# Kernel tuning notes

Hardware: AMD Instinct MI355X
Metric: run time of the kernel (lower is better)

## Reference

```python
import jax, jax.numpy as jnp
import numpy as np

N_PATCHES = 10
PATCH = 100
RECEPTIVE_FIELD = 0
N_SCALES = 2


def setup_inputs() -> dict:
    key = jax.random.key(0)
    k1, k2, k3, k4 = jax.random.split(key, 4)
    B, HL, WL, HH, WH = 8, 112, 112, 1024, 1024
    x_lows = jax.random.normal(k1, (N_SCALES, B, HL, WL, 3), jnp.float32)
    x_highs = jax.random.normal(k2, (N_SCALES, B, HH, WH, 3), jnp.float32)
    ats_map = jax.random.uniform(k3, (B, HL, WL), jnp.float32)
    ats_index = jax.random.randint(k4, (B, HL, WL), 0, N_SCALES).astype(jnp.int32)
    scales = jnp.array([1.0, 2.0], jnp.float32)
    return dict(x_lows=x_lows, x_highs=x_highs, ats_map=ats_map,
                ats_index=ats_index, scales=scales)


def _extract_patches(img, cy, cx):
    # img [H,W,3]; cy, cx [N] int32 -> [N,P,P,3] patch gather (vmapped dynamic_slice)
    def one(c):
        return jax.lax.dynamic_slice(img, (c[0], c[1], 0), (PATCH, PATCH, 3))
    return jax.vmap(one)(jnp.stack([cy, cx], axis=-1))


def _forward(x_lows, x_highs, ats_map, ats_index, scales):
    B, HL, WL = ats_map.shape
    HH, WH = x_highs.shape[2], x_highs.shape[3]
    # --- categorical sampling without replacement (Gumbel top-k) over flat attention
    att = ats_map.reshape(B, -1)
    att = att / att.sum(axis=-1, keepdims=True)
    gkey = jax.random.key(1)
    u = jax.random.uniform(gkey, (B, HL * WL))
    gumbel = -jnp.log(-jnp.log(u + 1e-10) + 1e-10)
    _, idx = jax.lax.top_k(jnp.log(att + 1e-10) + gumbel, N_PATCHES)  # [B,N]
    sampled_att = jnp.take_along_axis(att, idx, axis=1)               # [B,N]
    sy = (idx // WL).astype(jnp.float32)
    sx = (idx % WL).astype(jnp.float32)
    samples = jnp.stack([sy, sx], axis=-1)                            # [B,N,2]
    # per-sample scale routing: gather scale id at sampled locations
    res_index = jnp.take_along_axis(ats_index.reshape(B, -1), idx, axis=1)  # [B,N]
    # map low-res grid coords -> high-res top-left corners
    ratio = jnp.array([(HH - PATCH) / (HL - 1.0), (WH - PATCH) / (WL - 1.0)], jnp.float32)
    hi_max = jnp.array([HH - PATCH, WH - PATCH], jnp.int32)
    patches = jnp.zeros((B, N_PATCHES, PATCH, PATCH, 3), jnp.float32)
    samples_out = samples
    for s in range(N_SCALES):  # small static loop over scales (mirrors original)
        coords = samples / scales[s]                                   # divide both dims by scale
        corner = jnp.clip(jnp.round(coords * ratio).astype(jnp.int32), 0, hi_max)
        patches_s = jax.vmap(_extract_patches)(x_highs[s], corner[..., 0], corner[..., 1])
        mask = (res_index == s)                                        # [B,N]
        patches = jnp.where(mask[..., None, None, None], patches_s, patches)
        samples_out = jnp.where(mask[..., None], coords, samples_out)
    offsets = jnp.zeros_like(samples) + RECEPTIVE_FIELD / 2.0
    return patches, sampled_att, offsets, samples_out


def reference(x_lows, x_highs, ats_map, ats_index, scales):
    return _forward(x_lows, x_highs, ats_map, ats_index, scales)
```

## Files before the change

kernel.cpp:

```cpp
#include <hip/hip_runtime.h>
#include <math.h>

#define NPATCHES 10
#define PATCH    100
#define NSCALES  2
#define BB       8
#define HL       112
#define WL       112
#define HH       1024
#define WH       1024
#define HW       (HL*WL)
#define WSLICE   784
#define NW       16

__device__ __forceinline__ unsigned rotl32(unsigned x, unsigned r){
  return (x << r) | (x >> (32u - r));
}

__device__ __forceinline__ void threefry2x32_key01(unsigned x0, unsigned x1,
                                                   unsigned &o0, unsigned &o1){
  const unsigned ks0 = 0u;
  const unsigned ks1 = 1u;
  const unsigned ks2 = 0x1BD11BDAu ^ ks0 ^ ks1;
  unsigned a = x0 + ks0;
  unsigned b = x1 + ks1;
#define TF_RND(r) { a += b; b = rotl32(b, (r)); b ^= a; }
  TF_RND(13u) TF_RND(15u) TF_RND(26u) TF_RND(6u)
  a += ks1; b += ks2 + 1u;
  TF_RND(17u) TF_RND(29u) TF_RND(16u) TF_RND(24u)
  a += ks2; b += ks0 + 2u;
  TF_RND(13u) TF_RND(15u) TF_RND(26u) TF_RND(6u)
  a += ks0; b += ks1 + 3u;
  TF_RND(17u) TF_RND(29u) TF_RND(16u) TF_RND(24u)
  a += ks1; b += ks2 + 4u;
  TF_RND(13u) TF_RND(15u) TF_RND(26u) TF_RND(6u)
  a += ks2; b += ks0 + 5u;
#undef TF_RND
  o0 = a; o1 = b;
}

__global__ __launch_bounds__(1024)
void msp_topk_kernel(const float* __restrict__ ats_map,
                     const int*   __restrict__ ats_index,
                     const float* __restrict__ scales,
                     float* __restrict__ out,
                     int*   __restrict__ ws)
{
  __shared__ float swv[NW];
  __shared__ float cand_v[NW * NPATCHES];
  __shared__ int   cand_i[NW * NPATCHES];
  __shared__ float s_sum;
  __shared__ int   sel[NPATCHES];

  const int b = blockIdx.x;
  const int t = threadIdx.x;
  const int w = t >> 6;
  const int l = t & 63;
  const int base = w * WSLICE;
  const float* am = ats_map + (size_t)b * HW;

  float a[13];
  float ps = 0.0f;
  #pragma unroll
  for (int j = 0; j < 13; ++j){
    const int off = l + 64 * j;
    float x = 0.0f;
    if (off < WSLICE) x = am[base + off];
    a[j] = x;
    ps += x;
  }
  for (int d = 32; d > 0; d >>= 1) ps += __shfl_down(ps, d, 64);
  if (l == 0) swv[w] = ps;
  __syncthreads();
  if (t == 0){
    float s = 0.0f;
    for (int k = 0; k < NW; ++k) s += swv[k];
    s_sum = s;
  }
  __syncthreads();
  const float S = s_sum;

  #pragma unroll
  for (int j = 0; j < 13; ++j){
    const int off = l + 64 * j;
    const int i = base + off;
    unsigned o0, o1;
    threefry2x32_key01(0u, (unsigned)(b * HW + i), o0, o1);
    const unsigned bits = o0 ^ o1;
    const float u = __uint_as_float((bits >> 9) | 0x3f800000u) - 1.0f;
    const float g = -logf(-logf(u + 1e-10f) + 1e-10f);
    const float att = a[j] / S;
    const float sc = logf(att + 1e-10f) + g;
    a[j] = (off < WSLICE) ? sc : -INFINITY;
  }

  float lv = -INFINITY; int lj = 0;
  #pragma unroll
  for (int j = 0; j < 13; ++j) if (a[j] > lv){ lv = a[j]; lj = j; }

  for (int n = 0; n < NPATCHES; ++n){
    float bv = lv;
    int   bi = (lv == -INFINITY) ? 0x7fffffff : (base + l + 64 * lj);
    for (int d = 32; d > 0; d >>= 1){
      const float v2 = __shfl_down(bv, d, 64);
      const int   i2 = __shfl_down(bi, d, 64);
      if (v2 > bv || (v2 == bv && i2 < bi)){ bv = v2; bi = i2; }
    }
    bv = __shfl(bv, 0, 64);
    bi = __shfl(bi, 0, 64);
    if (l == 0){ cand_v[w * NPATCHES + n] = bv; cand_i[w * NPATCHES + n] = bi; }
    const int rel = bi - base;
    if (bi != 0x7fffffff && (rel & 63) == l){
      a[rel >> 6] = -INFINITY;
      lv = -INFINITY; lj = 0;
      #pragma unroll
      for (int j = 0; j < 13; ++j) if (a[j] > lv){ lv = a[j]; lj = j; }
    }
  }
  __syncthreads();

  if (w == 0){
    float mv[3]; int mi[3];
    #pragma unroll
    for (int c = 0; c < 3; ++c){
      const int id = l + 64 * c;
      if (id < NW * NPATCHES){ mv[c] = cand_v[id]; mi[c] = cand_i[id]; }
      else { mv[c] = -INFINITY; mi[c] = 0x7fffffff; }
    }
    float cv = -INFINITY; int ci = 0x7fffffff;
    #pragma unroll
    for (int c = 0; c < 3; ++c)
      if (mv[c] > cv || (mv[c] == cv && mi[c] < ci)){ cv = mv[c]; ci = mi[c]; }

    for (int n = 0; n < NPATCHES; ++n){
      float bv = cv; int bi = ci;
      for (int d = 32; d > 0; d >>= 1){
        const float v2 = __shfl_down(bv, d, 64);
        const int   i2 = __shfl_down(bi, d, 64);
        if (v2 > bv || (v2 == bv && i2 < bi)){ bv = v2; bi = i2; }
      }
      bv = __shfl(bv, 0, 64);
      bi = __shfl(bi, 0, 64);
      if (l == 0) sel[n] = bi;
      bool had = false;
      #pragma unroll
      for (int c = 0; c < 3; ++c) if (mi[c] == bi && mv[c] == bv){ mv[c] = -INFINITY; had = true; }
      if (had){
        cv = -INFINITY; ci = 0x7fffffff;
        #pragma unroll
        for (int c = 0; c < 3; ++c)
          if (mv[c] > cv || (mv[c] == cv && mi[c] < ci)){ cv = mv[c]; ci = mi[c]; }
      }
    }
  }
  __syncthreads();

  if (t < NPATCHES){
    const int n = t;
    const int idx = sel[n];
    const float att = am[idx] / S;
    const int iy = idx / WL;
    const float sy = (float)iy;
    const float sx = (float)(idx - iy * WL);
    const int si = ats_index[(size_t)b * HW + idx];
    const float sc = scales[si];
    const float cy = sy / sc;
    const float cx = sx / sc;
    const float ratio = (float)(924.0 / 111.0);
    int corner_y = (int)rintf(cy * ratio);
    int corner_x = (int)rintf(cx * ratio);
    corner_y = min(max(corner_y, 0), HH - PATCH);
    corner_x = min(max(corner_x, 0), WH - PATCH);

    float* out_att = out + (size_t)BB * NPATCHES * PATCH * PATCH * 3;
    float* out_off = out_att + BB * NPATCHES;
    float* out_smp = out_off + BB * NPATCHES * 2;
    out_att[b * NPATCHES + n] = att;
    out_off[(b * NPATCHES + n) * 2 + 0] = 0.0f;
    out_off[(b * NPATCHES + n) * 2 + 1] = 0.0f;
    out_smp[(b * NPATCHES + n) * 2 + 0] = cy;
    out_smp[(b * NPATCHES + n) * 2 + 1] = cx;

    int* wsp = ws + (b * NPATCHES + n) * 4;
    wsp[0] = corner_y; wsp[1] = corner_x; wsp[2] = si; wsp[3] = 0;
  }
}

__global__ __launch_bounds__(256)
void msp_gather_kernel(const float* __restrict__ x_highs,
                       const int*   __restrict__ ws,
                       float* __restrict__ out)
{
  const int pn    = blockIdx.x;
  const int chunk = blockIdx.y;
  const int t = threadIdx.x;
  const int* w = ws + pn * 4;
  const int cy = w[0], cx = w[1], s = w[2];
  const int b = pn / NPATCHES;
  const float* src = x_highs + (size_t)(s * BB + b) * HH * (WH * 3);
  float* dst = out + (size_t)pn * (PATCH * PATCH * 3);
  const int begin = chunk * 20 * PATCH * 3;
  const int end   = begin + 20 * PATCH * 3;
  for (int f = begin + t; f < end; f += 256){
    const int row = f / (PATCH * 3);
    const int col = f - row * (PATCH * 3);
    dst[f] = src[(size_t)(cy + row) * (WH * 3) + (size_t)cx * 3 + col];
  }
}

extern "C" void kernel_launch(void* const* d_in, const int* in_sizes, int n_in,
                              void* d_out, int out_size, void* d_ws, size_t ws_size,
                              hipStream_t stream)
{
  const float* x_highs   = (const float*)d_in[1];
  const float* ats_map   = (const float*)d_in[2];
  const int*   ats_index = (const int*)d_in[3];
  const float* scales    = (const float*)d_in[4];
  float* out = (float*)d_out;
  int*   ws  = (int*)d_ws;

  hipLaunchKernelGGL(msp_topk_kernel, dim3(BB), dim3(1024), 0, stream,
                     ats_map, ats_index, scales, out, ws);
  hipLaunchKernelGGL(msp_gather_kernel, dim3(BB * NPATCHES, 5), dim3(256), 0, stream,
                     x_highs, ws, out);
}
```

Baseline: 40.61 us.

## Fuse top-k sampling and patch gather into one kernel per patch

Merges the top-k selection kernel and the patch-gather kernel into a single launch with one 1024-thread block per (batch, patch). Each block redundantly recomputes the Gumbel top-k for its batch, then copies only its own patch using 4-wide stores. This removes a second launch and the workspace round trip, at the cost of running the top-k computation ten times over (once per patch) and having fewer gather blocks.

```diff
diff --git a/kernel.cpp b/kernel.cpp
--- a/kernel.cpp
+++ b/kernel.cpp
@@ -3,7 +3,6 @@
 
 #define NPATCHES 10
 #define PATCH    100
-#define NSCALES  2
 #define BB       8
 #define HL       112
 #define WL       112
@@ -40,22 +39,25 @@
 }
 
 __global__ __launch_bounds__(1024)
-void msp_topk_kernel(const float* __restrict__ ats_map,
-                     const int*   __restrict__ ats_index,
-                     const float* __restrict__ scales,
-                     float* __restrict__ out,
-                     int*   __restrict__ ws)
+void msp_fused_kernel(const float* __restrict__ x_highs,
+                      const float* __restrict__ ats_map,
+                      const int*   __restrict__ ats_index,
+                      const float* __restrict__ scales,
+                      float* __restrict__ out)
 {
   __shared__ float swv[NW];
   __shared__ float cand_v[NW * NPATCHES];
   __shared__ int   cand_i[NW * NPATCHES];
   __shared__ float s_sum;
   __shared__ int   sel[NPATCHES];
-
-  const int b = blockIdx.x;
-  const int t = threadIdx.x;
-  const int w = t >> 6;
-  const int l = t & 63;
+  __shared__ int   c_cy, c_cx, c_si;
+
+  const int pn = blockIdx.x;
+  const int b  = pn / NPATCHES;
+  const int n  = pn - b * NPATCHES;
+  const int t  = threadIdx.x;
+  const int w  = t >> 6;
+  const int l  = t & 63;
   const int base = w * WSLICE;
   const float* am = ats_map + (size_t)b * HW;
 
@@ -98,7 +100,7 @@
   #pragma unroll
   for (int j = 0; j < 13; ++j) if (a[j] > lv){ lv = a[j]; lj = j; }
 
-  for (int n = 0; n < NPATCHES; ++n){
+  for (int k = 0; k < NPATCHES; ++k){
     float bv = lv;
     int   bi = (lv == -INFINITY) ? 0x7fffffff : (base + l + 64 * lj);
     for (int d = 32; d > 0; d >>= 1){
@@ -108,7 +110,7 @@
     }
     bv = __shfl(bv, 0, 64);
     bi = __shfl(bi, 0, 64);
-    if (l == 0){ cand_v[w * NPATCHES + n] = bv; cand_i[w * NPATCHES + n] = bi; }
+    if (l == 0){ cand_v[w * NPATCHES + k] = bv; cand_i[w * NPATCHES + k] = bi; }
     const int rel = bi - base;
     if (bi != 0x7fffffff && (rel & 63) == l){
       a[rel >> 6] = -INFINITY;
@@ -132,7 +134,7 @@
     for (int c = 0; c < 3; ++c)
       if (mv[c] > cv || (mv[c] == cv && mi[c] < ci)){ cv = mv[c]; ci = mi[c]; }
 
-    for (int n = 0; n < NPATCHES; ++n){
+    for (int k = 0; k < NPATCHES; ++k){
       float bv = cv; int bi = ci;
       for (int d = 32; d > 0; d >>= 1){
         const float v2 = __shfl_down(bv, d, 64);
@@ -141,7 +143,7 @@
       }
       bv = __shfl(bv, 0, 64);
       bi = __shfl(bi, 0, 64);
-      if (l == 0) sel[n] = bi;
+      if (l == 0) sel[k] = bi;
       bool had = false;
       #pragma unroll
       for (int c = 0; c < 3; ++c) if (mi[c] == bi && mv[c] == bv){ mv[c] = -INFINITY; had = true; }
@@ -155,8 +157,7 @@
   }
   __syncthreads();
 
-  if (t < NPATCHES){
-    const int n = t;
+  if (t == 0){
     const int idx = sel[n];
     const float att = am[idx] / S;
     const int iy = idx / WL;
@@ -164,47 +165,36 @@
     const float sx = (float)(idx - iy * WL);
     const int si = ats_index[(size_t)b * HW + idx];
     const float sc = scales[si];
-    const float cy = sy / sc;
-    const float cx = sx / sc;
+    const float cyf = sy / sc;
+    const float cxf = sx / sc;
     const float ratio = (float)(924.0 / 111.0);
-    int corner_y = (int)rintf(cy * ratio);
-    int corner_x = (int)rintf(cx * ratio);
+    int corner_y = (int)rintf(cyf * ratio);
+    int corner_x = (int)rintf(cxf * ratio);
     corner_y = min(max(corner_y, 0), HH - PATCH);
     corner_x = min(max(corner_x, 0), WH - PATCH);
 
     float* out_att = out + (size_t)BB * NPATCHES * PATCH * PATCH * 3;
     float* out_off = out_att + BB * NPATCHES;
     float* out_smp = out_off + BB * NPATCHES * 2;
-    out_att[b * NPATCHES + n] = att;
-    out_off[(b * NPATCHES + n) * 2 + 0] = 0.0f;
-    out_off[(b * NPATCHES + n) * 2 + 1] = 0.0f;
-    out_smp[(b * NPATCHES + n) * 2 + 0] = cy;
-    out_smp[(b * NPATCHES + n) * 2 + 1] = cx;
-
-    int* wsp = ws + (b * NPATCHES + n) * 4;
-    wsp[0] = corner_y; wsp[1] = corner_x; wsp[2] = si; wsp[3] = 0;
-  }
-}
-
-__global__ __launch_bounds__(256)
-void msp_gather_kernel(const float* __restrict__ x_highs,
-                       const int*   __restrict__ ws,
-                       float* __restrict__ out)
-{
-  const int pn    = blockIdx.x;
-  const int chunk = blockIdx.y;
-  const int t = threadIdx.x;
-  const int* w = ws + pn * 4;
-  const int cy = w[0], cx = w[1], s = w[2];
-  const int b = pn / NPATCHES;
-  const float* src = x_highs + (size_t)(s * BB + b) * HH * (WH * 3);
+    out_att[pn] = att;
+    out_off[pn * 2 + 0] = 0.0f;
+    out_off[pn * 2 + 1] = 0.0f;
+    out_smp[pn * 2 + 0] = cyf;
+    out_smp[pn * 2 + 1] = cxf;
+
+    c_cy = corner_y; c_cx = corner_x; c_si = si;
+  }
+  __syncthreads();
+
+  const int cy = c_cy, cx = c_cx, s = c_si;
+  const float* src = x_highs + (size_t)(s * BB + b) * ((size_t)HH * (WH * 3));
   float* dst = out + (size_t)pn * (PATCH * PATCH * 3);
-  const int begin = chunk * 20 * PATCH * 3;
-  const int end   = begin + 20 * PATCH * 3;
-  for (int f = begin + t; f < end; f += 256){
-    const int row = f / (PATCH * 3);
-    const int col = f - row * (PATCH * 3);
-    dst[f] = src[(size_t)(cy + row) * (WH * 3) + (size_t)cx * 3 + col];
+  for (int f = t * 4; f < PATCH * PATCH * 3; f += 4096){
+    const int row = f / 300;
+    const int col = f - row * 300;
+    const float* sp = src + (size_t)(cy + row) * (WH * 3) + (size_t)cx * 3 + col;
+    float4 v = make_float4(sp[0], sp[1], sp[2], sp[3]);
+    *reinterpret_cast<float4*>(dst + f) = v;
   }
 }
 
@@ -217,10 +207,7 @@
   const int*   ats_index = (const int*)d_in[3];
   const float* scales    = (const float*)d_in[4];
   float* out = (float*)d_out;
-  int*   ws  = (int*)d_ws;
-
-  hipLaunchKernelGGL(msp_topk_kernel, dim3(BB), dim3(1024), 0, stream,
-                     ats_map, ats_index, scales, out, ws);
-  hipLaunchKernelGGL(msp_gather_kernel, dim3(BB * NPATCHES, 5), dim3(256), 0, stream,
-                     x_highs, ws, out);
-}
+
+  hipLaunchKernelGGL(msp_fused_kernel, dim3(BB * NPATCHES), dim3(1024), 0, stream,
+                     x_highs, ats_map, ats_index, scales, out);
+}
```

Measured after the change: 38.59 us. -5.0%, faster.
